# Kernel tuning notes

Hardware: AMD Instinct MI355X
Metric: run time of the kernel (lower is better)

## Reference

```python
import jax, jax.numpy as jnp
import numpy as np

ROUTING_ITERS = 3

def squash(t, axis=-1):
    sq_norm = jnp.sum(t * t, axis=axis, keepdims=True)
    scale = sq_norm / (1.0 + sq_norm)
    return scale * t / jnp.sqrt(sq_norm + 1e-8)

def setup_inputs() -> dict:
    key = jax.random.key(0)
    k1, k2 = jax.random.split(key)
    B, N, I, J, O = 64, 2048, 16, 32, 32
    x = jax.random.normal(k1, (B, N, I), dtype=jnp.float32)
    weights = jax.random.normal(k2, (N, J, O, I), dtype=jnp.float32) * 0.1
    return {"x": x, "weights": weights}

def reference(x, weights):
    B, N, _ = x.shape
    J = weights.shape[1]
    # predictions u_{j|i}: [B, N, J, O]
    predictions = jnp.einsum('bni,njoi->bnjo', x, weights)
    b = jnp.zeros((B, N, J, 1), dtype=x.dtype)
    v = None
    for i in range(ROUTING_ITERS):
        c = jax.nn.softmax(b, axis=2)                      # coupling over capsules J
        s = jnp.sum(predictions * c, axis=1, keepdims=True)  # [B,1,J,O]
        v = squash(s, axis=-1)
        if i < ROUTING_ITERS - 1:
            agreement = jnp.sum(predictions * v, axis=-1, keepdims=True)  # [B,N,J,1]
            b = b + agreement
    return jnp.squeeze(v, axis=1)  # [B, J, O]
```

## Files before the change

kernel.cpp:

```cpp
#include <hip/hip_runtime.h>
#include <hip/hip_bf16.h>

#define B_ 64
#define N_ 2048
#define I_ 16
#define J_ 32
#define O_ 32
#define JO_ 1024

typedef __attribute__((ext_vector_type(8))) short bf16x8;
typedef __attribute__((ext_vector_type(16))) float f32x16;
typedef unsigned short u16;
typedef unsigned int u32;

__device__ __forceinline__ float bf2f(u16 u) {
  union { u32 i; float f; } c; c.i = ((u32)u) << 16; return c.f;
}
__device__ __forceinline__ u16 f2bf(float f) {
  union { float f; u32 i; } c; c.f = f;
  u32 r = (c.i + 0x7fffu + ((c.i >> 16) & 1u)) >> 16;
  return (u16)r;
}
__device__ __forceinline__ u32 pack2(float a, float b) {
  return (u32)f2bf(a) | ((u32)f2bf(b) << 16);
}
__device__ __forceinline__ u32 scale2(u32 p, float cv) {
  return pack2(bf2f((u16)(p & 0xffffu)) * cv, bf2f((u16)(p >> 16)) * cv);
}

__global__ __launch_bounds__(256) void xconv_kernel(
    const float* __restrict__ xf, u16* __restrict__ xt)
{
  const int idx = blockIdx.x * 256 + threadIdx.x;
  const int b = idx >> 11, n = idx & 2047;
  const float4* sp = (const float4*)(xf + (size_t)idx * 16);
  float4 f0 = sp[0], f1 = sp[1], f2 = sp[2], f3 = sp[3];
  uint4 d0, d1;
  d0.x = pack2(f0.x, f0.y); d0.y = pack2(f0.z, f0.w);
  d0.z = pack2(f1.x, f1.y); d0.w = pack2(f1.z, f1.w);
  d1.x = pack2(f2.x, f2.y); d1.y = pack2(f2.z, f2.w);
  d1.z = pack2(f3.x, f3.y); d1.w = pack2(f3.z, f3.w);
  uint4* dp = (uint4*)(xt + ((size_t)n * 64 + b) * 16);
  dp[0] = d0; dp[1] = d1;
}

__global__ __launch_bounds__(256) void wconv_kernel(
    const float* __restrict__ wf, u16* __restrict__ wb)
{
  const size_t row = (size_t)blockIdx.x * 256 + threadIdx.x;
  const float4* sp = (const float4*)(wf + row * 16);
  float4 f0 = sp[0], f1 = sp[1], f2 = sp[2], f3 = sp[3];
  uint4 d0, d1;
  d0.x = pack2(f0.x, f0.y); d0.y = pack2(f0.z, f0.w);
  d0.z = pack2(f1.x, f1.y); d0.w = pack2(f1.z, f1.w);
  d1.x = pack2(f2.x, f2.y); d1.y = pack2(f2.z, f2.w);
  d1.z = pack2(f3.x, f3.y); d1.w = pack2(f3.z, f3.w);
  uint4* dp = (uint4*)(wb + row * 16);
  dp[0] = d0; dp[1] = d1;
}

#define SF_NPW 16

__global__ __launch_bounds__(256, 4) void sf_kernel(
    const u16* __restrict__ xt, const u16* __restrict__ wb,
    const u16* __restrict__ ct, float* __restrict__ s_sum, int uniform)
{
  __shared__ float red[4][2048];
  const int tid = threadIdx.x;
  const int wave = tid >> 6, lane = tid & 63;
  const int l31 = lane & 31, h = lane >> 5;
  const int j = blockIdx.x, split = blockIdx.y;
  const int n0 = (split * 4 + wave) * SF_NPW;
  f32x16 acc0 = {0.f, 0.f, 0.f, 0.f, 0.f, 0.f, 0.f, 0.f,
                 0.f, 0.f, 0.f, 0.f, 0.f, 0.f, 0.f, 0.f};
  f32x16 acc1 = acc0;

  #pragma unroll 4
  for (int i = 0; i < SF_NPW; ++i) {
    const int n = n0 + i;
    bf16x8 wfr = *(const bf16x8*)(wb + ((size_t)n * JO_ + j * 32 + l31) * 16 + h * 8);
    bf16x8 x0 = *(const bf16x8*)(xt + ((size_t)n * 64 + l31) * 16 + h * 8);
    bf16x8 x1 = *(const bf16x8*)(xt + ((size_t)n * 64 + 32 + l31) * 16 + h * 8);
    if (!uniform) {
      const float cv0 = bf2f(ct[((size_t)j * N_ + n) * 64 + l31]);
      const float cv1 = bf2f(ct[((size_t)j * N_ + n) * 64 + 32 + l31]);
      union { bf16x8 v; u32 u[4]; } a, b2;
      a.v = x0; b2.v = x1;
      a.u[0] = scale2(a.u[0], cv0); a.u[1] = scale2(a.u[1], cv0);
      a.u[2] = scale2(a.u[2], cv0); a.u[3] = scale2(a.u[3], cv0);
      b2.u[0] = scale2(b2.u[0], cv1); b2.u[1] = scale2(b2.u[1], cv1);
      b2.u[2] = scale2(b2.u[2], cv1); b2.u[3] = scale2(b2.u[3], cv1);
      x0 = a.v; x1 = b2.v;
    }
    acc0 = __builtin_amdgcn_mfma_f32_32x32x16_bf16(wfr, x0, acc0, 0, 0, 0);
    acc1 = __builtin_amdgcn_mfma_f32_32x32x16_bf16(wfr, x1, acc1, 0, 0, 0);
  }
  #pragma unroll
  for (int r = 0; r < 16; ++r) {
    const int o = (r & 3) + 8 * (r >> 2) + 4 * h;
    red[wave][o * 64 + l31] = acc0[r];
    red[wave][o * 64 + 32 + l31] = acc1[r];
  }
  __syncthreads();
  #pragma unroll
  for (int k = 0; k < 8; ++k) {
    const int idx = tid + 256 * k;
    const int o = idx >> 6, b = idx & 63;
    const float sum = red[0][idx] + red[1][idx] + red[2][idx] + red[3][idx];
    atomicAdd(&s_sum[(size_t)(j * 32 + o) * 64 + b], sum);
  }
}

__global__ __launch_bounds__(64) void r_kernel(
    const float* __restrict__ s_sum, float* __restrict__ v,
    const float* __restrict__ vprev, u16* __restrict__ v4,
    float* __restrict__ out, int mode, float scale)
{
  const int tid = threadIdx.x;
  const int jj = tid >> 5, o = tid & 31;
  const int b = blockIdx.x >> 4, jg = blockIdx.x & 15;
  const int j = jg * 2 + jj;
  const float s = s_sum[(size_t)(j * 32 + o) * 64 + b] * scale;
  float sq = s * s;
  #pragma unroll
  for (int m = 16; m >= 1; m >>= 1) sq += __shfl_xor(sq, m, 64);
  const float sc = sq / (1.f + sq) * rsqrtf(sq + 1e-8f);
  const float vv = sc * s;
  const size_t off = (size_t)b * JO_ + j * 32 + o;
  const int g = o >> 3, hh = (o >> 2) & 1, rr = o & 3;
  const size_t v4off = ((((size_t)j * 4 + g) * 2 + hh) * 64 + b) * 4 + rr;
  if (mode == 0) { v[off] = vv; v4[v4off] = f2bf(vv); }
  else if (mode == 1) { v4[v4off] = f2bf(vv + vprev[off]); }
  else { out[off] = vv; }
}

__global__ __launch_bounds__(256, 4) void a_kernel(
    const u16* __restrict__ xt, const u16* __restrict__ wb,
    const u16* __restrict__ v4, u16* __restrict__ ct)
{
  __shared__ float lgs[2][64][33];
  const int tid = threadIdx.x;
  const int wave = tid >> 6, lane = tid & 63;
  const int l31 = lane & 31, h = lane >> 5;
  const int nl = wave >> 1, th = wave & 1;
  const int n = blockIdx.x * 2 + nl;
  const f32x16 zero16 = {0.f, 0.f, 0.f, 0.f, 0.f, 0.f, 0.f, 0.f,
                         0.f, 0.f, 0.f, 0.f, 0.f, 0.f, 0.f, 0.f};

  const bf16x8 x0 = *(const bf16x8*)(xt + ((size_t)n * 64 + l31) * 16 + h * 8);
  const bf16x8 x1 = *(const bf16x8*)(xt + ((size_t)n * 64 + 32 + l31) * 16 + h * 8);

  #pragma unroll 2
  for (int tt = 0; tt < 16; ++tt) {
    const int t = th * 16 + tt;
    const bf16x8 wfr =
        *(const bf16x8*)(wb + ((size_t)n * JO_ + t * 32 + l31) * 16 + h * 8);
    f32x16 p0 = __builtin_amdgcn_mfma_f32_32x32x16_bf16(wfr, x0, zero16, 0, 0, 0);
    f32x16 p1 = __builtin_amdgcn_mfma_f32_32x32x16_bf16(wfr, x1, zero16, 0, 0, 0);
    float s0 = 0.f, s1 = 0.f;
    #pragma unroll
    for (int g = 0; g < 4; ++g) {
      const int vbase = (((t * 4 + g) * 2 + h) * 64) * 4;
      const ushort4 va = *(const ushort4*)(v4 + vbase + l31 * 4);
      const ushort4 vb = *(const ushort4*)(v4 + vbase + (32 + l31) * 4);
      s0 += p0[g * 4 + 0] * bf2f(va.x) + p0[g * 4 + 1] * bf2f(va.y)
          + p0[g * 4 + 2] * bf2f(va.z) + p0[g * 4 + 3] * bf2f(va.w);
      s1 += p1[g * 4 + 0] * bf2f(vb.x) + p1[g * 4 + 1] * bf2f(vb.y)
          + p1[g * 4 + 2] * bf2f(vb.z) + p1[g * 4 + 3] * bf2f(vb.w);
    }
    s0 += __shfl_xor(s0, 32, 64);
    s1 += __shfl_xor(s1, 32, 64);
    lgs[nl][lane][t] = h ? s1 : s0;
  }
  __syncthreads();

  if (tid < 128) {
    const int nl2 = tid >> 6, b = tid & 63;
    const int n2 = blockIdx.x * 2 + nl2;
    float lv[32];
    float mx = -1e30f;
    #pragma unroll
    for (int t = 0; t < 32; ++t) {
      lv[t] = lgs[nl2][b][t];
      mx = fmaxf(mx, lv[t]);
    }
    float sm = 0.f;
    #pragma unroll
    for (int t = 0; t < 32; ++t) { lv[t] = __expf(lv[t] - mx); sm += lv[t]; }
    const float inv = 1.f / sm;
    #pragma unroll
    for (int t = 0; t < 32; ++t) {
      ct[((size_t)t * N_ + n2) * 64 + b] = f2bf(lv[t] * inv);
    }
  }
}

extern "C" void kernel_launch(void* const* d_in, const int* in_sizes, int n_in,
                              void* d_out, int out_size, void* d_ws, size_t ws_size,
                              hipStream_t stream) {
  const float* x = (const float*)d_in[0];
  const float* w = (const float*)d_in[1];
  float* out = (float*)d_out;
  char* ws = (char*)d_ws;
  u16*   wb    = (u16*)ws;
  u16*   ct    = (u16*)(ws + (size_t)64 * 1024 * 1024);
  u16*   xt    = (u16*)(ws + (size_t)72 * 1024 * 1024);
  float* s_sum = (float*)(ws + (size_t)76 * 1024 * 1024);
  float* v0    = (float*)(ws + (size_t)76 * 1024 * 1024 + 262144);
  u16*   v4    = (u16*)(ws + (size_t)76 * 1024 * 1024 + 2 * 262144);

  const size_t s_bytes = (size_t)JO_ * B_ * sizeof(float);
  dim3 sfg(32, 32), sfb(256);
  dim3 ag(1024), ab(256);
  dim3 rg(1024), rb(64);

  xconv_kernel<<<dim3(512), dim3(256), 0, stream>>>(x, xt);
  wconv_kernel<<<dim3(8192), dim3(256), 0, stream>>>(w, wb);
  hipMemsetAsync(s_sum, 0, s_bytes, stream);
  sf_kernel<<<sfg, sfb, 0, stream>>>(xt, wb, ct, s_sum, 1);
  r_kernel<<<rg, rb, 0, stream>>>(s_sum, v0, v0, v4, out, 0, 0.03125f);
  a_kernel<<<ag, ab, 0, stream>>>(xt, wb, v4, ct);
  hipMemsetAsync(s_sum, 0, s_bytes, stream);
  sf_kernel<<<sfg, sfb, 0, stream>>>(xt, wb, ct, s_sum, 0);
  r_kernel<<<rg, rb, 0, stream>>>(s_sum, v0, v0, v4, out, 1, 1.0f);
  a_kernel<<<ag, ab, 0, stream>>>(xt, wb, v4, ct);
  hipMemsetAsync(s_sum, 0, s_bytes, stream);
  sf_kernel<<<sfg, sfb, 0, stream>>>(xt, wb, ct, s_sum, 0);
  r_kernel<<<rg, rb, 0, stream>>>(s_sum, v0, v0, v4, out, 2, 1.0f);
}
```

Measured before the change: 332.2 us.

## Fuse weight conversion into first routing pass and replace atomics with split partials

The separate fp32-to-bf16 weight conversion kernel is folded into the first s-accumulation pass, which converts weights on the fly, writes the bf16 copy and feeds the MFMAs directly. This saves one full read of the 128MB fp32 weights. Atomic accumulation plus memsets is replaced by per-split partial buffers that the squash kernel sums. Packed bf16 conversion instructions replace manual rounding. The agreement kernel now handles one capsule row per block with coalesced coupling stores through shared memory. The trade-offs are extra partial-buffer traffic and a 32-way reduction in r_kernel.

Result: no change. 331.0 us (-0.3%).

```diff
diff --git a/kernel.cpp b/kernel.cpp
--- a/kernel.cpp
+++ b/kernel.cpp
@@ -7,6 +7,7 @@
 #define J_ 32
 #define O_ 32
 #define JO_ 1024
+#define SPLITS 32
 
 typedef __attribute__((ext_vector_type(8))) short bf16x8;
 typedef __attribute__((ext_vector_type(16))) float f32x16;
@@ -21,11 +22,15 @@
   u32 r = (c.i + 0x7fffu + ((c.i >> 16) & 1u)) >> 16;
   return (u16)r;
 }
-__device__ __forceinline__ u32 pack2(float a, float b) {
-  return (u32)f2bf(a) | ((u32)f2bf(b) << 16);
-}
-__device__ __forceinline__ u32 scale2(u32 p, float cv) {
-  return pack2(bf2f((u16)(p & 0xffffu)) * cv, bf2f((u16)(p >> 16)) * cv);
+__device__ __forceinline__ u32 pack2_pk(float lo, float hi) {
+  u32 r;
+  asm("v_cvt_pk_bf16_f32 %0, %1, %2" : "=v"(r) : "v"(lo), "v"(hi));
+  return r;
+}
+__device__ __forceinline__ u32 scale2_pk(u32 p, float cv) {
+  union { u32 i; float f; } lo, hi;
+  lo.i = p << 16; hi.i = p & 0xffff0000u;
+  return pack2_pk(lo.f * cv, hi.f * cv);
 }
 
 __global__ __launch_bounds__(256) void xconv_kernel(
@@ -36,34 +41,19 @@
   const float4* sp = (const float4*)(xf + (size_t)idx * 16);
   float4 f0 = sp[0], f1 = sp[1], f2 = sp[2], f3 = sp[3];
   uint4 d0, d1;
-  d0.x = pack2(f0.x, f0.y); d0.y = pack2(f0.z, f0.w);
-  d0.z = pack2(f1.x, f1.y); d0.w = pack2(f1.z, f1.w);
-  d1.x = pack2(f2.x, f2.y); d1.y = pack2(f2.z, f2.w);
-  d1.z = pack2(f3.x, f3.y); d1.w = pack2(f3.z, f3.w);
+  d0.x = pack2_pk(f0.x, f0.y); d0.y = pack2_pk(f0.z, f0.w);
+  d0.z = pack2_pk(f1.x, f1.y); d0.w = pack2_pk(f1.z, f1.w);
+  d1.x = pack2_pk(f2.x, f2.y); d1.y = pack2_pk(f2.z, f2.w);
+  d1.z = pack2_pk(f3.x, f3.y); d1.w = pack2_pk(f3.z, f3.w);
   uint4* dp = (uint4*)(xt + ((size_t)n * 64 + b) * 16);
   dp[0] = d0; dp[1] = d1;
 }
 
-__global__ __launch_bounds__(256) void wconv_kernel(
-    const float* __restrict__ wf, u16* __restrict__ wb)
-{
-  const size_t row = (size_t)blockIdx.x * 256 + threadIdx.x;
-  const float4* sp = (const float4*)(wf + row * 16);
-  float4 f0 = sp[0], f1 = sp[1], f2 = sp[2], f3 = sp[3];
-  uint4 d0, d1;
-  d0.x = pack2(f0.x, f0.y); d0.y = pack2(f0.z, f0.w);
-  d0.z = pack2(f1.x, f1.y); d0.w = pack2(f1.z, f1.w);
-  d1.x = pack2(f2.x, f2.y); d1.y = pack2(f2.z, f2.w);
-  d1.z = pack2(f3.x, f3.y); d1.w = pack2(f3.z, f3.w);
-  uint4* dp = (uint4*)(wb + row * 16);
-  dp[0] = d0; dp[1] = d1;
-}
-
 #define SF_NPW 16
 
-__global__ __launch_bounds__(256, 4) void sf_kernel(
-    const u16* __restrict__ xt, const u16* __restrict__ wb,
-    const u16* __restrict__ ct, float* __restrict__ s_sum, int uniform)
+__global__ __launch_bounds__(256, 4) void wsf_kernel(
+    const float* __restrict__ wf, u16* __restrict__ wb,
+    const u16* __restrict__ xt, float* __restrict__ s_part)
 {
   __shared__ float red[4][2048];
   const int tid = threadIdx.x;
@@ -78,22 +68,18 @@
   #pragma unroll 4
   for (int i = 0; i < SF_NPW; ++i) {
     const int n = n0 + i;
-    bf16x8 wfr = *(const bf16x8*)(wb + ((size_t)n * JO_ + j * 32 + l31) * 16 + h * 8);
-    bf16x8 x0 = *(const bf16x8*)(xt + ((size_t)n * 64 + l31) * 16 + h * 8);
-    bf16x8 x1 = *(const bf16x8*)(xt + ((size_t)n * 64 + 32 + l31) * 16 + h * 8);
-    if (!uniform) {
-      const float cv0 = bf2f(ct[((size_t)j * N_ + n) * 64 + l31]);
-      const float cv1 = bf2f(ct[((size_t)j * N_ + n) * 64 + 32 + l31]);
-      union { bf16x8 v; u32 u[4]; } a, b2;
-      a.v = x0; b2.v = x1;
-      a.u[0] = scale2(a.u[0], cv0); a.u[1] = scale2(a.u[1], cv0);
-      a.u[2] = scale2(a.u[2], cv0); a.u[3] = scale2(a.u[3], cv0);
-      b2.u[0] = scale2(b2.u[0], cv1); b2.u[1] = scale2(b2.u[1], cv1);
-      b2.u[2] = scale2(b2.u[2], cv1); b2.u[3] = scale2(b2.u[3], cv1);
-      x0 = a.v; x1 = b2.v;
-    }
-    acc0 = __builtin_amdgcn_mfma_f32_32x32x16_bf16(wfr, x0, acc0, 0, 0, 0);
-    acc1 = __builtin_amdgcn_mfma_f32_32x32x16_bf16(wfr, x1, acc1, 0, 0, 0);
+    const size_t row = (size_t)n * JO_ + j * 32 + l31;
+    const float* wsrc = wf + row * 16 + h * 8;
+    const float4 f0 = *(const float4*)(wsrc);
+    const float4 f1 = *(const float4*)(wsrc + 4);
+    union { uint4 u4; bf16x8 bv; } wd;
+    wd.u4.x = pack2_pk(f0.x, f0.y); wd.u4.y = pack2_pk(f0.z, f0.w);
+    wd.u4.z = pack2_pk(f1.x, f1.y); wd.u4.w = pack2_pk(f1.z, f1.w);
+    *(uint4*)(wb + row * 16 + h * 8) = wd.u4;
+    const bf16x8 x0 = *(const bf16x8*)(xt + ((size_t)n * 64 + l31) * 16 + h * 8);
+    const bf16x8 x1 = *(const bf16x8*)(xt + ((size_t)n * 64 + 32 + l31) * 16 + h * 8);
+    acc0 = __builtin_amdgcn_mfma_f32_32x32x16_bf16(wd.bv, x0, acc0, 0, 0, 0);
+    acc1 = __builtin_amdgcn_mfma_f32_32x32x16_bf16(wd.bv, x1, acc1, 0, 0, 0);
   }
   #pragma unroll
   for (int r = 0; r < 16; ++r) {
@@ -102,17 +88,61 @@
     red[wave][o * 64 + 32 + l31] = acc1[r];
   }
   __syncthreads();
+  float* dst = s_part + (size_t)split * (JO_ * B_) + (size_t)j * 32 * 64;
   #pragma unroll
   for (int k = 0; k < 8; ++k) {
     const int idx = tid + 256 * k;
-    const int o = idx >> 6, b = idx & 63;
-    const float sum = red[0][idx] + red[1][idx] + red[2][idx] + red[3][idx];
-    atomicAdd(&s_sum[(size_t)(j * 32 + o) * 64 + b], sum);
+    dst[idx] = red[0][idx] + red[1][idx] + red[2][idx] + red[3][idx];
+  }
+}
+
+__global__ __launch_bounds__(256, 4) void sf_kernel(
+    const u16* __restrict__ xt, const u16* __restrict__ wb,
+    const u16* __restrict__ ct, float* __restrict__ s_part)
+{
+  __shared__ float red[4][2048];
+  const int tid = threadIdx.x;
+  const int wave = tid >> 6, lane = tid & 63;
+  const int l31 = lane & 31, h = lane >> 5;
+  const int j = blockIdx.x, split = blockIdx.y;
+  const int n0 = (split * 4 + wave) * SF_NPW;
+  f32x16 acc0 = {0.f, 0.f, 0.f, 0.f, 0.f, 0.f, 0.f, 0.f,
+                 0.f, 0.f, 0.f, 0.f, 0.f, 0.f, 0.f, 0.f};
+  f32x16 acc1 = acc0;
+
+  #pragma unroll 4
+  for (int i = 0; i < SF_NPW; ++i) {
+    const int n = n0 + i;
+    bf16x8 wfr = *(const bf16x8*)(wb + ((size_t)n * JO_ + j * 32 + l31) * 16 + h * 8);
+    union { bf16x8 v; u32 u[4]; } a, b2;
+    a.v = *(const bf16x8*)(xt + ((size_t)n * 64 + l31) * 16 + h * 8);
+    b2.v = *(const bf16x8*)(xt + ((size_t)n * 64 + 32 + l31) * 16 + h * 8);
+    const float cv0 = bf2f(ct[((size_t)j * N_ + n) * 64 + l31]);
+    const float cv1 = bf2f(ct[((size_t)j * N_ + n) * 64 + 32 + l31]);
+    a.u[0] = scale2_pk(a.u[0], cv0); a.u[1] = scale2_pk(a.u[1], cv0);
+    a.u[2] = scale2_pk(a.u[2], cv0); a.u[3] = scale2_pk(a.u[3], cv0);
+    b2.u[0] = scale2_pk(b2.u[0], cv1); b2.u[1] = scale2_pk(b2.u[1], cv1);
+    b2.u[2] = scale2_pk(b2.u[2], cv1); b2.u[3] = scale2_pk(b2.u[3], cv1);
+    acc0 = __builtin_amdgcn_mfma_f32_32x32x16_bf16(wfr, a.v, acc0, 0, 0, 0);
+    acc1 = __builtin_amdgcn_mfma_f32_32x32x16_bf16(wfr, b2.v, acc1, 0, 0, 0);
+  }
+  #pragma unroll
+  for (int r = 0; r < 16; ++r) {
+    const int o = (r & 3) + 8 * (r >> 2) + 4 * h;
+    red[wave][o * 64 + l31] = acc0[r];
+    red[wave][o * 64 + 32 + l31] = acc1[r];
+  }
+  __syncthreads();
+  float* dst = s_part + (size_t)split * (JO_ * B_) + (size_t)j * 32 * 64;
+  #pragma unroll
+  for (int k = 0; k < 8; ++k) {
+    const int idx = tid + 256 * k;
+    dst[idx] = red[0][idx] + red[1][idx] + red[2][idx] + red[3][idx];
   }
 }
 
 __global__ __launch_bounds__(64) void r_kernel(
-    const float* __restrict__ s_sum, float* __restrict__ v,
+    const float* __restrict__ s_part, float* __restrict__ v,
     const float* __restrict__ vprev, u16* __restrict__ v4,
     float* __restrict__ out, int mode, float scale)
 {
@@ -120,7 +150,11 @@
   const int jj = tid >> 5, o = tid & 31;
   const int b = blockIdx.x >> 4, jg = blockIdx.x & 15;
   const int j = jg * 2 + jj;
-  const float s = s_sum[(size_t)(j * 32 + o) * 64 + b] * scale;
+  const size_t off_jo = (size_t)(j * 32 + o) * 64 + b;
+  float s = 0.f;
+  #pragma unroll
+  for (int k = 0; k < SPLITS; ++k) s += s_part[(size_t)k * (JO_ * B_) + off_jo];
+  s *= scale;
   float sq = s * s;
   #pragma unroll
   for (int m = 16; m >= 1; m >>= 1) sq += __shfl_xor(sq, m, 64);
@@ -134,16 +168,15 @@
   else { out[off] = vv; }
 }
 
-__global__ __launch_bounds__(256, 4) void a_kernel(
+__global__ __launch_bounds__(256, 6) void a_kernel(
     const u16* __restrict__ xt, const u16* __restrict__ wb,
     const u16* __restrict__ v4, u16* __restrict__ ct)
 {
-  __shared__ float lgs[2][64][33];
+  __shared__ float lgs[64][33];
   const int tid = threadIdx.x;
   const int wave = tid >> 6, lane = tid & 63;
   const int l31 = lane & 31, h = lane >> 5;
-  const int nl = wave >> 1, th = wave & 1;
-  const int n = blockIdx.x * 2 + nl;
+  const int n = blockIdx.x;
   const f32x16 zero16 = {0.f, 0.f, 0.f, 0.f, 0.f, 0.f, 0.f, 0.f,
                          0.f, 0.f, 0.f, 0.f, 0.f, 0.f, 0.f, 0.f};
 
@@ -151,8 +184,8 @@
   const bf16x8 x1 = *(const bf16x8*)(xt + ((size_t)n * 64 + 32 + l31) * 16 + h * 8);
 
   #pragma unroll 2
-  for (int tt = 0; tt < 16; ++tt) {
-    const int t = th * 16 + tt;
+  for (int tt = 0; tt < 8; ++tt) {
+    const int t = wave * 8 + tt;
     const bf16x8 wfr =
         *(const bf16x8*)(wb + ((size_t)n * JO_ + t * 32 + l31) * 16 + h * 8);
     f32x16 p0 = __builtin_amdgcn_mfma_f32_32x32x16_bf16(wfr, x0, zero16, 0, 0, 0);
@@ -170,28 +203,30 @@
     }
     s0 += __shfl_xor(s0, 32, 64);
     s1 += __shfl_xor(s1, 32, 64);
-    lgs[nl][lane][t] = h ? s1 : s0;
-  }
-  __syncthreads();
-
-  if (tid < 128) {
-    const int nl2 = tid >> 6, b = tid & 63;
-    const int n2 = blockIdx.x * 2 + nl2;
+    lgs[lane][t] = h ? s1 : s0;
+  }
+  __syncthreads();
+
+  if (tid < 64) {
+    const int b = tid;
     float lv[32];
     float mx = -1e30f;
     #pragma unroll
-    for (int t = 0; t < 32; ++t) {
-      lv[t] = lgs[nl2][b][t];
-      mx = fmaxf(mx, lv[t]);
-    }
+    for (int t = 0; t < 32; ++t) { lv[t] = lgs[b][t]; mx = fmaxf(mx, lv[t]); }
     float sm = 0.f;
     #pragma unroll
     for (int t = 0; t < 32; ++t) { lv[t] = __expf(lv[t] - mx); sm += lv[t]; }
     const float inv = 1.f / sm;
     #pragma unroll
-    for (int t = 0; t < 32; ++t) {
-      ct[((size_t)t * N_ + n2) * 64 + b] = f2bf(lv[t] * inv);
-    }
+    for (int t = 0; t < 32; ++t) lgs[b][t] = lv[t] * inv;
+  }
+  __syncthreads();
+
+  #pragma unroll
+  for (int k = 0; k < 8; ++k) {
+    const int idx = k * 256 + tid;
+    const int t = idx >> 6, b = idx & 63;
+    ct[((size_t)t * N_ + n) * 64 + b] = f2bf(lgs[b][t]);
   }
 }
 
@@ -202,29 +237,24 @@
   const float* w = (const float*)d_in[1];
   float* out = (float*)d_out;
   char* ws = (char*)d_ws;
-  u16*   wb    = (u16*)ws;
-  u16*   ct    = (u16*)(ws + (size_t)64 * 1024 * 1024);
-  u16*   xt    = (u16*)(ws + (size_t)72 * 1024 * 1024);
-  float* s_sum = (float*)(ws + (size_t)76 * 1024 * 1024);
-  float* v0    = (float*)(ws + (size_t)76 * 1024 * 1024 + 262144);
-  u16*   v4    = (u16*)(ws + (size_t)76 * 1024 * 1024 + 2 * 262144);
-
-  const size_t s_bytes = (size_t)JO_ * B_ * sizeof(float);
-  dim3 sfg(32, 32), sfb(256);
-  dim3 ag(1024), ab(256);
+  u16*   wb     = (u16*)ws;
+  u16*   ct     = (u16*)(ws + (size_t)64 * 1024 * 1024);
+  u16*   xt     = (u16*)(ws + (size_t)72 * 1024 * 1024);
+  float* s_part = (float*)(ws + (size_t)76 * 1024 * 1024);
+  float* v0     = (float*)(ws + (size_t)84 * 1024 * 1024);
+  u16*   v4     = (u16*)(ws + (size_t)84 * 1024 * 1024 + 262144);
+
+  dim3 sfg(32, SPLITS), sfb(256);
+  dim3 ag(2048), ab(256);
   dim3 rg(1024), rb(64);
 
   xconv_kernel<<<dim3(512), dim3(256), 0, stream>>>(x, xt);
-  wconv_kernel<<<dim3(8192), dim3(256), 0, stream>>>(w, wb);
-  hipMemsetAsync(s_sum, 0, s_bytes, stream);
-  sf_kernel<<<sfg, sfb, 0, stream>>>(xt, wb, ct, s_sum, 1);
-  r_kernel<<<rg, rb, 0, stream>>>(s_sum, v0, v0, v4, out, 0, 0.03125f);
+  wsf_kernel<<<sfg, sfb, 0, stream>>>(w, wb, xt, s_part);
+  r_kernel<<<rg, rb, 0, stream>>>(s_part, v0, v0, v4, out, 0, 0.03125f);
   a_kernel<<<ag, ab, 0, stream>>>(xt, wb, v4, ct);
-  hipMemsetAsync(s_sum, 0, s_bytes, stream);
-  sf_kernel<<<sfg, sfb, 0, stream>>>(xt, wb, ct, s_sum, 0);
-  r_kernel<<<rg, rb, 0, stream>>>(s_sum, v0, v0, v4, out, 1, 1.0f);
+  sf_kernel<<<sfg, sfb, 0, stream>>>(xt, wb, ct, s_part);
+  r_kernel<<<rg, rb, 0, stream>>>(s_part, v0, v0, v4, out, 1, 1.0f);
   a_kernel<<<ag, ab, 0, stream>>>(xt, wb, v4, ct);
-  hipMemsetAsync(s_sum, 0, s_bytes, stream);
-  sf_kernel<<<sfg, sfb, 0, stream>>>(xt, wb, ct, s_sum, 0);
-  r_kernel<<<rg, rb, 0, stream>>>(s_sum, v0, v0, v4, out, 2, 1.0f);
-}
+  sf_kernel<<<sfg, sfb, 0, stream>>>(xt, wb, ct, s_part);
+  r_kernel<<<rg, rb, 0, stream>>>(s_part, v0, v0, v4, out, 2, 1.0f);
+}
```
